# Performance work log

Hardware: AMD Instinct MI355X
Metric: run time of the kernel (lower is better)

Reference implementation:

```python
import jax, jax.numpy as jnp
import numpy as np

B = 64            # number of graphs
NODES_PER_G = 64  # real nodes per graph
N_MAX = 128       # max_num_nodes (dense padding)
NT = B * NODES_PER_G   # 4096 total nodes
E = 65536         # edges (and pairs)
H = 64            # hidden_dim
D_NODE = 32
POLY = 16


def setup_inputs() -> dict:
    key = jax.random.key(0)
    ks = jax.random.split(key, 12)
    node_x = jax.random.normal(ks[0], (NT, D_NODE), dtype=jnp.float32)
    loop_x = jax.random.normal(ks[1], (NT, POLY), dtype=jnp.float32)
    edge_attr = jax.random.normal(ks[2], (E, D_NODE), dtype=jnp.float32)
    pair_x = jax.random.normal(ks[3], (E, POLY), dtype=jnp.float32)
    W_node = jax.random.normal(ks[4], (D_NODE, H), dtype=jnp.float32) / np.sqrt(D_NODE)
    W_loop = jax.random.normal(ks[5], (POLY, H), dtype=jnp.float32) / np.sqrt(POLY)
    W_edge = jax.random.normal(ks[6], (D_NODE, H), dtype=jnp.float32) / np.sqrt(D_NODE)
    W_pair = jax.random.normal(ks[7], (POLY, H), dtype=jnp.float32) / np.sqrt(POLY)
    # sorted graph assignment: 64 nodes per graph
    batch = (jnp.arange(NT, dtype=jnp.int32) // NODES_PER_G).astype(jnp.int32)
    # intra-graph edges: global index = graph*NODES_PER_G + local
    epg = E // B  # edges per graph
    eg = (jnp.arange(E, dtype=jnp.int32) // epg)
    e_loc = jax.random.randint(ks[8], (2, E), 0, NODES_PER_G, dtype=jnp.int32)
    edge_index = eg[None, :] * NODES_PER_G + e_loc
    p_loc = jax.random.randint(ks[9], (2, E), 0, NODES_PER_G, dtype=jnp.int32)
    pair_index = eg[None, :] * NODES_PER_G + p_loc
    return {
        "node_x": node_x, "loop_x": loop_x, "edge_attr": edge_attr, "pair_x": pair_x,
        "W_node": W_node, "W_loop": W_loop, "W_edge": W_edge, "W_pair": W_pair,
        "batch": batch, "edge_index": edge_index, "pair_index": pair_index,
    }


def _positions(batch):
    # position of each node within its graph (to_dense_batch semantics)
    counts = jax.ops.segment_sum(jnp.ones_like(batch), batch, num_segments=B)
    starts = jnp.concatenate([jnp.zeros((1,), counts.dtype), jnp.cumsum(counts)[:-1]])
    return jnp.arange(batch.shape[0], dtype=batch.dtype) - starts[batch].astype(batch.dtype)


def _to_dense_adj(index, batch, pos, h):
    b = batch[index[0]]
    r = pos[index[0]]
    c = pos[index[1]]
    dense = jnp.zeros((B, N_MAX, N_MAX, H), dtype=h.dtype)
    return dense.at[b, r, c].add(h)  # duplicates are summed, as in to_dense_adj


def reference(node_x, loop_x, edge_attr, pair_x, W_node, W_loop, W_edge, W_pair,
              batch, edge_index, pair_index):
    pos = _positions(batch)
    # node + loop encoders (linear), then scatter to dense batch [B, N, H]
    node_h = node_x @ W_node + loop_x @ W_loop
    dense_node_h = jnp.zeros((B, N_MAX, H), dtype=node_h.dtype).at[batch, pos].set(node_h)
    dense_node_mask = jnp.zeros((B, N_MAX), dtype=bool).at[batch, pos].set(True)
    # permute (0,2,1) -> [B, H, N], then diag_embed -> [B, H, N, N]
    dnh = jnp.transpose(dense_node_h, (0, 2, 1))
    ar = jnp.arange(N_MAX)
    dense_diag_h = jnp.zeros((B, H, N_MAX, N_MAX), dtype=dnh.dtype).at[:, :, ar, ar].set(dnh)
    # edge + pair encoders, scatter to dense adjacency [B, N, N, H]
    edge_h = edge_attr @ W_edge
    pair_h = pair_x @ W_pair
    dense_pair = _to_dense_adj(edge_index, batch, pos, edge_h) \
               + _to_dense_adj(pair_index, batch, pos, pair_h)
    # permute (0,3,1,2) -> [B, H, N, N], add diagonal node features
    dense_pair_h = jnp.transpose(dense_pair, (0, 3, 1, 2)) + dense_diag_h
    return dense_pair_h, dense_node_mask
```

## Files before the change

kernel.cpp:

```cpp
#include <hip/hip_runtime.h>

#define NTOT  4096
#define NG    64
#define NMAXD 128
#define HD    64
#define NEDGE 65536
#define EPG   (NEDGE / NG)
#define NPG   (NTOT / NG)

typedef float f4 __attribute__((ext_vector_type(4)));

__device__ __forceinline__ int lowb(const int* __restrict__ batch, int key) {
  int lo = 0, hi = NTOT;
  while (lo < hi) { const int mid = (lo + hi) >> 1;
    if (batch[mid] < key) lo = mid + 1; else hi = mid; }
  return lo;
}

__global__ __launch_bounds__(256) void prep_all_kernel(
    const int* __restrict__ eI, const int* __restrict__ pI,
    const int* __restrict__ batch,
    int* __restrict__ rcE, int* __restrict__ rcP, int* __restrict__ rcN,
    int* __restrict__ counts) {
  const int i = blockIdx.x * 256 + threadIdx.x;
  if (i < NEDGE) {
    const int n0 = eI[i], n1 = eI[NEDGE + i];
    const int b0 = batch[n0], b1 = batch[n1];
    rcE[i] = (b0 << 16) | ((n0 - lowb(batch, b0)) << 8) | (n1 - lowb(batch, b1));
  } else if (i < 2 * NEDGE) {
    const int j = i - NEDGE;
    const int n0 = pI[j], n1 = pI[NEDGE + j];
    const int b0 = batch[n0], b1 = batch[n1];
    rcP[j] = (b0 << 16) | ((n0 - lowb(batch, b0)) << 8) | (n1 - lowb(batch, b1));
  } else if (i < 2 * NEDGE + NTOT) {
    const int j = i - 2 * NEDGE;
    const int b = batch[j];
    const int p = j - lowb(batch, b);
    rcN[j] = (b << 16) | (p << 8) | p;
  } else if (i < 2 * NEDGE + NTOT + NG) {
    const int g = i - 2 * NEDGE - NTOT;
    counts[g] = lowb(batch, g + 1) - lowb(batch, g);
  }
}

#define HQ 4
#define SCT 512
__global__ __launch_bounds__(SCT) void fused_scatter_kernel(
    const float* __restrict__ node_x, const float* __restrict__ loop_x,
    const float* __restrict__ edge_attr, const float* __restrict__ pair_x,
    const float* __restrict__ Wn, const float* __restrict__ Wl,
    const float* __restrict__ We, const float* __restrict__ Wp,
    const int* __restrict__ rcE, const int* __restrict__ rcP,
    const int* __restrict__ rcN, const int* __restrict__ counts,
    float* __restrict__ out, float* __restrict__ mask) {
  __shared__ float acc[HQ * 4096];
  __shared__ f4 WcE[32];
  __shared__ f4 WcP[16];
  __shared__ f4 WcN[48];

  const int tid = threadIdx.x;
  const int d  = (int)blockIdx.x;
  const int g  = ((d & 7) << 3) | ((d >> 3) & 7);
  const int h0 = (d >> 6) * HQ;

  if (tid < 32)       WcE[tid]            = *(const f4*)&We[tid * HD + h0];
  else if (tid < 48)  WcP[tid - 32]       = *(const f4*)&Wp[(tid - 32) * HD + h0];
  else if (tid < 80)  WcN[tid - 48]       = *(const f4*)&Wn[(tid - 48) * HD + h0];
  else if (tid < 96)  WcN[32 + tid - 80]  = *(const f4*)&Wl[(tid - 80) * HD + h0];
  for (int i = tid; i < HQ * 1024; i += SCT) ((f4*)acc)[i] = (f4)(0.f);
  __syncthreads();

  const int wid = tid >> 6;
  if (wid >= 4) {
    const int tz = tid - 256;
#pragma unroll
    for (int t = 0; t < HQ; ++t) {
      f4* plane = (f4*)(out + ((size_t)g * HD + h0 + t) * NMAXD * NMAXD);
#pragma unroll
      for (int k = 0; k < 4; ++k) {
        const int idx = tz + k * 256;
        plane[(idx >> 4) * 32 + 16 + (idx & 15)] = (f4)(0.f);
      }
#pragma unroll
      for (int k = 0; k < 8; ++k)
        plane[2048 + tz + k * 256] = (f4)(0.f);
    }
    if (h0 == 0) {
      const int cg = counts[g];
      for (int i = tz; i < NMAXD; i += 256)
        mask[(size_t)g * NMAXD + i] = (i < cg) ? 1.0f : 0.0f;
    }
  } else {
#pragma unroll
    for (int k = 0; k < 4; ++k) {
      const int j = g * EPG + tid + k * 256;
      const f4* xr = (const f4*)(edge_attr + (size_t)j * 32);
      f4 d4 = (f4)(0.f);
#pragma unroll
      for (int k4 = 0; k4 < 8; ++k4) {
        const f4 x = xr[k4];
#pragma unroll
        for (int u = 0; u < 4; ++u) d4 += x[u] * WcE[k4 * 4 + u];
      }
      const int code = rcE[j];
      const int b = code >> 16, r = (code >> 8) & 255, c = code & 255;
      if (b == g && r < 64 && c < 64) {
        const int a = r * 64 + c;
        unsafeAtomicAdd(&acc[a], d4.x);          unsafeAtomicAdd(&acc[4096 + a], d4.y);
        unsafeAtomicAdd(&acc[8192 + a], d4.z);   unsafeAtomicAdd(&acc[12288 + a], d4.w);
      } else {
        unsafeAtomicAdd(&out[(((size_t)b * HD + h0 + 0) * NMAXD + r) * NMAXD + c], d4.x);
        unsafeAtomicAdd(&out[(((size_t)b * HD + h0 + 1) * NMAXD + r) * NMAXD + c], d4.y);
        unsafeAtomicAdd(&out[(((size_t)b * HD + h0 + 2) * NMAXD + r) * NMAXD + c], d4.z);
        unsafeAtomicAdd(&out[(((size_t)b * HD + h0 + 3) * NMAXD + r) * NMAXD + c], d4.w);
      }
    }

#pragma unroll
    for (int k = 0; k < 4; ++k) {
      const int j = g * EPG + tid + k * 256;
      const f4* xr = (const f4*)(pair_x + (size_t)j * 16);
      f4 d4 = (f4)(0.f);
#pragma unroll
      for (int k4 = 0; k4 < 4; ++k4) {
        const f4 x = xr[k4];
#pragma unroll
        for (int u = 0; u < 4; ++u) d4 += x[u] * WcP[k4 * 4 + u];
      }
      const int code = rcP[j];
      const int b = code >> 16, r = (code >> 8) & 255, c = code & 255;
      if (b == g && r < 64 && c < 64) {
        const int a = r * 64 + c;
        unsafeAtomicAdd(&acc[a], d4.x);          unsafeAtomicAdd(&acc[4096 + a], d4.y);
        unsafeAtomicAdd(&acc[8192 + a], d4.z);   unsafeAtomicAdd(&acc[12288 + a], d4.w);
      } else {
        unsafeAtomicAdd(&out[(((size_t)b * HD + h0 + 0) * NMAXD + r) * NMAXD + c], d4.x);
        unsafeAtomicAdd(&out[(((size_t)b * HD + h0 + 1) * NMAXD + r) * NMAXD + c], d4.y);
        unsafeAtomicAdd(&out[(((size_t)b * HD + h0 + 2) * NMAXD + r) * NMAXD + c], d4.z);
        unsafeAtomicAdd(&out[(((size_t)b * HD + h0 + 3) * NMAXD + r) * NMAXD + c], d4.w);
      }
    }

    if (tid < NPG) {
      const int j = g * NPG + tid;
      const f4* xr = (const f4*)(node_x + (size_t)j * 32);
      const f4* lr = (const f4*)(loop_x + (size_t)j * 16);
      f4 d4 = (f4)(0.f);
#pragma unroll
      for (int k4 = 0; k4 < 8; ++k4) {
        const f4 x = xr[k4];
#pragma unroll
        for (int u = 0; u < 4; ++u) d4 += x[u] * WcN[k4 * 4 + u];
      }
#pragma unroll
      for (int k4 = 0; k4 < 4; ++k4) {
        const f4 x = lr[k4];
#pragma unroll
        for (int u = 0; u < 4; ++u) d4 += x[u] * WcN[32 + k4 * 4 + u];
      }
      const int code = rcN[j];
      const int b = code >> 16, r = (code >> 8) & 255, c = code & 255;
      if (b == g && r < 64 && c < 64) {
        const int a = r * 64 + c;
        unsafeAtomicAdd(&acc[a], d4.x);          unsafeAtomicAdd(&acc[4096 + a], d4.y);
        unsafeAtomicAdd(&acc[8192 + a], d4.z);   unsafeAtomicAdd(&acc[12288 + a], d4.w);
      } else {
        unsafeAtomicAdd(&out[(((size_t)b * HD + h0 + 0) * NMAXD + r) * NMAXD + c], d4.x);
        unsafeAtomicAdd(&out[(((size_t)b * HD + h0 + 1) * NMAXD + r) * NMAXD + c], d4.y);
        unsafeAtomicAdd(&out[(((size_t)b * HD + h0 + 2) * NMAXD + r) * NMAXD + c], d4.z);
        unsafeAtomicAdd(&out[(((size_t)b * HD + h0 + 3) * NMAXD + r) * NMAXD + c], d4.w);
      }
    }
  }
  __syncthreads();

#pragma unroll
  for (int t = 0; t < HQ; ++t) {
    f4* plane = (f4*)(out + ((size_t)g * HD + h0 + t) * NMAXD * NMAXD);
#pragma unroll
    for (int k = 0; k < 2; ++k) {
      const int idx = tid + k * SCT;
      const int r = idx >> 4, c4 = idx & 15;
      plane[r * 32 + c4] = *(const f4*)&acc[t * 4096 + r * 64 + c4 * 4];
    }
  }
}

extern "C" void kernel_launch(void* const* d_in, const int* in_sizes, int n_in,
                              void* d_out, int out_size, void* d_ws, size_t ws_size,
                              hipStream_t stream) {
  const float* node_x    = (const float*)d_in[0];
  const float* loop_x    = (const float*)d_in[1];
  const float* edge_attr = (const float*)d_in[2];
  const float* pair_x    = (const float*)d_in[3];
  const float* W_node    = (const float*)d_in[4];
  const float* W_loop    = (const float*)d_in[5];
  const float* W_edge    = (const float*)d_in[6];
  const float* W_pair    = (const float*)d_in[7];
  const int*   batch     = (const int*)d_in[8];
  const int*   edge_index = (const int*)d_in[9];
  const int*   pair_index = (const int*)d_in[10];

  float* out  = (float*)d_out;
  float* mask = out + (size_t)NG * HD * NMAXD * NMAXD;

  int* rcE    = (int*)d_ws;
  int* rcP    = rcE + NEDGE;
  int* rcN    = rcP + NEDGE;
  int* counts = rcN + NTOT;

  const int prep_items = 2 * NEDGE + NTOT + NG;
  prep_all_kernel<<<(prep_items + 255) / 256, 256, 0, stream>>>(
      edge_index, pair_index, batch, rcE, rcP, rcN, counts);
  fused_scatter_kernel<<<NG * 16, SCT, 0, stream>>>(node_x, loop_x, edge_attr,
      pair_x, W_node, W_loop, W_edge, W_pair, rcE, rcP, rcN, counts, out, mask);
}
```

Measured before the change: 73.39 us.

## Move output zero-fill into prep kernel and use all threads for scatter

```diff
diff --git a/kernel.cpp b/kernel.cpp
--- a/kernel.cpp
+++ b/kernel.cpp
@@ -10,6 +10,10 @@
 
 typedef float f4 __attribute__((ext_vector_type(4)));
 
+#define NZBLK 2048
+#define PREP_ITEMS (2 * NEDGE + NTOT + NG)
+#define NPBLK ((PREP_ITEMS + 255) / 256)
+
 __device__ __forceinline__ int lowb(const int* __restrict__ batch, int key) {
   int lo = 0, hi = NTOT;
   while (lo < hi) { const int mid = (lo + hi) >> 1;
@@ -17,12 +21,30 @@
   return lo;
 }
 
-__global__ __launch_bounds__(256) void prep_all_kernel(
+__global__ __launch_bounds__(256) void zero_prep_kernel(
     const int* __restrict__ eI, const int* __restrict__ pI,
     const int* __restrict__ batch,
     int* __restrict__ rcE, int* __restrict__ rcP, int* __restrict__ rcN,
-    int* __restrict__ counts) {
-  const int i = blockIdx.x * 256 + threadIdx.x;
+    int* __restrict__ counts, float* __restrict__ out) {
+  const int blk = (int)blockIdx.x;
+  const int tid = threadIdx.x;
+
+  if (blk < NZBLK) {
+#pragma unroll
+    for (int t = 0; t < 2; ++t) {
+      f4* plane = (f4*)(out + (size_t)(blk * 2 + t) * (NMAXD * NMAXD));
+#pragma unroll
+      for (int k = 0; k < 8; ++k) plane[2048 + tid + k * 256] = (f4)(0.f);
+#pragma unroll
+      for (int k = 0; k < 4; ++k) {
+        const int i = tid + k * 256;
+        plane[(i >> 4) * 32 + 16 + (i & 15)] = (f4)(0.f);
+      }
+    }
+    return;
+  }
+
+  const int i = (blk - NZBLK) * 256 + tid;
   if (i < NEDGE) {
     const int n0 = eI[i], n1 = eI[NEDGE + i];
     const int b0 = batch[n0], b1 = batch[n1];
@@ -37,15 +59,15 @@
     const int b = batch[j];
     const int p = j - lowb(batch, b);
     rcN[j] = (b << 16) | (p << 8) | p;
-  } else if (i < 2 * NEDGE + NTOT + NG) {
+  } else if (i < PREP_ITEMS) {
     const int g = i - 2 * NEDGE - NTOT;
     counts[g] = lowb(batch, g + 1) - lowb(batch, g);
   }
 }
 
 #define HQ 4
-#define SCT 512
-__global__ __launch_bounds__(SCT) void fused_scatter_kernel(
+#define BT 512
+__global__ __launch_bounds__(BT) void acc_kernel(
     const float* __restrict__ node_x, const float* __restrict__ loop_x,
     const float* __restrict__ edge_attr, const float* __restrict__ pair_x,
     const float* __restrict__ Wn, const float* __restrict__ Wl,
@@ -67,109 +89,87 @@
   else if (tid < 48)  WcP[tid - 32]       = *(const f4*)&Wp[(tid - 32) * HD + h0];
   else if (tid < 80)  WcN[tid - 48]       = *(const f4*)&Wn[(tid - 48) * HD + h0];
   else if (tid < 96)  WcN[32 + tid - 80]  = *(const f4*)&Wl[(tid - 80) * HD + h0];
-  for (int i = tid; i < HQ * 1024; i += SCT) ((f4*)acc)[i] = (f4)(0.f);
+  for (int i = tid; i < HQ * 1024; i += BT) ((f4*)acc)[i] = (f4)(0.f);
   __syncthreads();
 
-  const int wid = tid >> 6;
-  if (wid >= 4) {
-    const int tz = tid - 256;
-#pragma unroll
-    for (int t = 0; t < HQ; ++t) {
-      f4* plane = (f4*)(out + ((size_t)g * HD + h0 + t) * NMAXD * NMAXD);
-#pragma unroll
-      for (int k = 0; k < 4; ++k) {
-        const int idx = tz + k * 256;
-        plane[(idx >> 4) * 32 + 16 + (idx & 15)] = (f4)(0.f);
-      }
-#pragma unroll
-      for (int k = 0; k < 8; ++k)
-        plane[2048 + tz + k * 256] = (f4)(0.f);
-    }
-    if (h0 == 0) {
-      const int cg = counts[g];
-      for (int i = tz; i < NMAXD; i += 256)
-        mask[(size_t)g * NMAXD + i] = (i < cg) ? 1.0f : 0.0f;
-    }
-  } else {
-#pragma unroll
-    for (int k = 0; k < 4; ++k) {
-      const int j = g * EPG + tid + k * 256;
-      const f4* xr = (const f4*)(edge_attr + (size_t)j * 32);
-      f4 d4 = (f4)(0.f);
-#pragma unroll
-      for (int k4 = 0; k4 < 8; ++k4) {
-        const f4 x = xr[k4];
-#pragma unroll
-        for (int u = 0; u < 4; ++u) d4 += x[u] * WcE[k4 * 4 + u];
-      }
-      const int code = rcE[j];
-      const int b = code >> 16, r = (code >> 8) & 255, c = code & 255;
-      if (b == g && r < 64 && c < 64) {
-        const int a = r * 64 + c;
-        unsafeAtomicAdd(&acc[a], d4.x);          unsafeAtomicAdd(&acc[4096 + a], d4.y);
-        unsafeAtomicAdd(&acc[8192 + a], d4.z);   unsafeAtomicAdd(&acc[12288 + a], d4.w);
-      } else {
-        unsafeAtomicAdd(&out[(((size_t)b * HD + h0 + 0) * NMAXD + r) * NMAXD + c], d4.x);
-        unsafeAtomicAdd(&out[(((size_t)b * HD + h0 + 1) * NMAXD + r) * NMAXD + c], d4.y);
-        unsafeAtomicAdd(&out[(((size_t)b * HD + h0 + 2) * NMAXD + r) * NMAXD + c], d4.z);
-        unsafeAtomicAdd(&out[(((size_t)b * HD + h0 + 3) * NMAXD + r) * NMAXD + c], d4.w);
-      }
-    }
-
-#pragma unroll
-    for (int k = 0; k < 4; ++k) {
-      const int j = g * EPG + tid + k * 256;
-      const f4* xr = (const f4*)(pair_x + (size_t)j * 16);
-      f4 d4 = (f4)(0.f);
-#pragma unroll
-      for (int k4 = 0; k4 < 4; ++k4) {
-        const f4 x = xr[k4];
-#pragma unroll
-        for (int u = 0; u < 4; ++u) d4 += x[u] * WcP[k4 * 4 + u];
-      }
-      const int code = rcP[j];
-      const int b = code >> 16, r = (code >> 8) & 255, c = code & 255;
-      if (b == g && r < 64 && c < 64) {
-        const int a = r * 64 + c;
-        unsafeAtomicAdd(&acc[a], d4.x);          unsafeAtomicAdd(&acc[4096 + a], d4.y);
-        unsafeAtomicAdd(&acc[8192 + a], d4.z);   unsafeAtomicAdd(&acc[12288 + a], d4.w);
-      } else {
-        unsafeAtomicAdd(&out[(((size_t)b * HD + h0 + 0) * NMAXD + r) * NMAXD + c], d4.x);
-        unsafeAtomicAdd(&out[(((size_t)b * HD + h0 + 1) * NMAXD + r) * NMAXD + c], d4.y);
-        unsafeAtomicAdd(&out[(((size_t)b * HD + h0 + 2) * NMAXD + r) * NMAXD + c], d4.z);
-        unsafeAtomicAdd(&out[(((size_t)b * HD + h0 + 3) * NMAXD + r) * NMAXD + c], d4.w);
-      }
-    }
-
-    if (tid < NPG) {
-      const int j = g * NPG + tid;
-      const f4* xr = (const f4*)(node_x + (size_t)j * 32);
-      const f4* lr = (const f4*)(loop_x + (size_t)j * 16);
-      f4 d4 = (f4)(0.f);
-#pragma unroll
-      for (int k4 = 0; k4 < 8; ++k4) {
-        const f4 x = xr[k4];
-#pragma unroll
-        for (int u = 0; u < 4; ++u) d4 += x[u] * WcN[k4 * 4 + u];
-      }
-#pragma unroll
-      for (int k4 = 0; k4 < 4; ++k4) {
-        const f4 x = lr[k4];
-#pragma unroll
-        for (int u = 0; u < 4; ++u) d4 += x[u] * WcN[32 + k4 * 4 + u];
-      }
-      const int code = rcN[j];
-      const int b = code >> 16, r = (code >> 8) & 255, c = code & 255;
-      if (b == g && r < 64 && c < 64) {
-        const int a = r * 64 + c;
-        unsafeAtomicAdd(&acc[a], d4.x);          unsafeAtomicAdd(&acc[4096 + a], d4.y);
-        unsafeAtomicAdd(&acc[8192 + a], d4.z);   unsafeAtomicAdd(&acc[12288 + a], d4.w);
-      } else {
-        unsafeAtomicAdd(&out[(((size_t)b * HD + h0 + 0) * NMAXD + r) * NMAXD + c], d4.x);
-        unsafeAtomicAdd(&out[(((size_t)b * HD + h0 + 1) * NMAXD + r) * NMAXD + c], d4.y);
-        unsafeAtomicAdd(&out[(((size_t)b * HD + h0 + 2) * NMAXD + r) * NMAXD + c], d4.z);
-        unsafeAtomicAdd(&out[(((size_t)b * HD + h0 + 3) * NMAXD + r) * NMAXD + c], d4.w);
-      }
+#pragma unroll
+  for (int k = 0; k < 2; ++k) {
+    const int j = g * EPG + tid + k * BT;
+    const f4* xr = (const f4*)(edge_attr + (size_t)j * 32);
+    f4 d4 = (f4)(0.f);
+#pragma unroll
+    for (int k4 = 0; k4 < 8; ++k4) {
+      const f4 x = xr[k4];
+#pragma unroll
+      for (int u = 0; u < 4; ++u) d4 += x[u] * WcE[k4 * 4 + u];
+    }
+    const int code = rcE[j];
+    const int b = code >> 16, r = (code >> 8) & 255, c = code & 255;
+    if (b == g && r < 64 && c < 64) {
+      const int a = r * 64 + c;
+      unsafeAtomicAdd(&acc[a], d4.x);          unsafeAtomicAdd(&acc[4096 + a], d4.y);
+      unsafeAtomicAdd(&acc[8192 + a], d4.z);   unsafeAtomicAdd(&acc[12288 + a], d4.w);
+    } else {
+      unsafeAtomicAdd(&out[(((size_t)b * HD + h0 + 0) * NMAXD + r) * NMAXD + c], d4.x);
+      unsafeAtomicAdd(&out[(((size_t)b * HD + h0 + 1) * NMAXD + r) * NMAXD + c], d4.y);
+      unsafeAtomicAdd(&out[(((size_t)b * HD + h0 + 2) * NMAXD + r) * NMAXD + c], d4.z);
+      unsafeAtomicAdd(&out[(((size_t)b * HD + h0 + 3) * NMAXD + r) * NMAXD + c], d4.w);
+    }
+  }
+
+#pragma unroll
+  for (int k = 0; k < 2; ++k) {
+    const int j = g * EPG + tid + k * BT;
+    const f4* xr = (const f4*)(pair_x + (size_t)j * 16);
+    f4 d4 = (f4)(0.f);
+#pragma unroll
+    for (int k4 = 0; k4 < 4; ++k4) {
+      const f4 x = xr[k4];
+#pragma unroll
+      for (int u = 0; u < 4; ++u) d4 += x[u] * WcP[k4 * 4 + u];
+    }
+    const int code = rcP[j];
+    const int b = code >> 16, r = (code >> 8) & 255, c = code & 255;
+    if (b == g && r < 64 && c < 64) {
+      const int a = r * 64 + c;
+      unsafeAtomicAdd(&acc[a], d4.x);          unsafeAtomicAdd(&acc[4096 + a], d4.y);
+      unsafeAtomicAdd(&acc[8192 + a], d4.z);   unsafeAtomicAdd(&acc[12288 + a], d4.w);
+    } else {
+      unsafeAtomicAdd(&out[(((size_t)b * HD + h0 + 0) * NMAXD + r) * NMAXD + c], d4.x);
+      unsafeAtomicAdd(&out[(((size_t)b * HD + h0 + 1) * NMAXD + r) * NMAXD + c], d4.y);
+      unsafeAtomicAdd(&out[(((size_t)b * HD + h0 + 2) * NMAXD + r) * NMAXD + c], d4.z);
+      unsafeAtomicAdd(&out[(((size_t)b * HD + h0 + 3) * NMAXD + r) * NMAXD + c], d4.w);
+    }
+  }
+
+  if (tid < NPG) {
+    const int j = g * NPG + tid;
+    const f4* xr = (const f4*)(node_x + (size_t)j * 32);
+    const f4* lr = (const f4*)(loop_x + (size_t)j * 16);
+    f4 d4 = (f4)(0.f);
+#pragma unroll
+    for (int k4 = 0; k4 < 8; ++k4) {
+      const f4 x = xr[k4];
+#pragma unroll
+      for (int u = 0; u < 4; ++u) d4 += x[u] * WcN[k4 * 4 + u];
+    }
+#pragma unroll
+    for (int k4 = 0; k4 < 4; ++k4) {
+      const f4 x = lr[k4];
+#pragma unroll
+      for (int u = 0; u < 4; ++u) d4 += x[u] * WcN[32 + k4 * 4 + u];
+    }
+    const int code = rcN[j];
+    const int b = code >> 16, r = (code >> 8) & 255, c = code & 255;
+    if (b == g && r < 64 && c < 64) {
+      const int a = r * 64 + c;
+      unsafeAtomicAdd(&acc[a], d4.x);          unsafeAtomicAdd(&acc[4096 + a], d4.y);
+      unsafeAtomicAdd(&acc[8192 + a], d4.z);   unsafeAtomicAdd(&acc[12288 + a], d4.w);
+    } else {
+      unsafeAtomicAdd(&out[(((size_t)b * HD + h0 + 0) * NMAXD + r) * NMAXD + c], d4.x);
+      unsafeAtomicAdd(&out[(((size_t)b * HD + h0 + 1) * NMAXD + r) * NMAXD + c], d4.y);
+      unsafeAtomicAdd(&out[(((size_t)b * HD + h0 + 2) * NMAXD + r) * NMAXD + c], d4.z);
+      unsafeAtomicAdd(&out[(((size_t)b * HD + h0 + 3) * NMAXD + r) * NMAXD + c], d4.w);
     }
   }
   __syncthreads();
@@ -179,11 +179,14 @@
     f4* plane = (f4*)(out + ((size_t)g * HD + h0 + t) * NMAXD * NMAXD);
 #pragma unroll
     for (int k = 0; k < 2; ++k) {
-      const int idx = tid + k * SCT;
+      const int idx = tid + k * BT;
       const int r = idx >> 4, c4 = idx & 15;
       plane[r * 32 + c4] = *(const f4*)&acc[t * 4096 + r * 64 + c4 * 4];
     }
   }
+
+  if (h0 == 0 && tid < NMAXD)
+    mask[(size_t)g * NMAXD + tid] = (tid < counts[g]) ? 1.0f : 0.0f;
 }
 
 extern "C" void kernel_launch(void* const* d_in, const int* in_sizes, int n_in,
@@ -209,9 +212,8 @@
   int* rcN    = rcP + NEDGE;
   int* counts = rcN + NTOT;
 
-  const int prep_items = 2 * NEDGE + NTOT + NG;
-  prep_all_kernel<<<(prep_items + 255) / 256, 256, 0, stream>>>(
-      edge_index, pair_index, batch, rcE, rcP, rcN, counts);
-  fused_scatter_kernel<<<NG * 16, SCT, 0, stream>>>(node_x, loop_x, edge_attr,
+  zero_prep_kernel<<<NZBLK + NPBLK, 256, 0, stream>>>(
+      edge_index, pair_index, batch, rcE, rcP, rcN, counts, out);
+  acc_kernel<<<NG * 16, BT, 0, stream>>>(node_x, loop_x, edge_attr,
       pair_x, W_node, W_loop, W_edge, W_pair, rcE, rcP, rcN, counts, out, mask);
 }
```

Result: slower. 98.80 us (+34.6%).

## Split edge dot-products across 4 lanes with shuffle reduction and rotated LDS planes

Applied to the files above, without the earlier changes.

```diff
diff --git a/kernel.cpp b/kernel.cpp
--- a/kernel.cpp
+++ b/kernel.cpp
@@ -9,6 +9,15 @@
 #define NPG   (NTOT / NG)
 
 typedef float f4 __attribute__((ext_vector_type(4)));
+
+#define ROT(a, s) (((a) + (s) * 8) & 4095)
+
+__device__ __forceinline__ f4 shfl_xor_f4(f4 v, int m) {
+  f4 r;
+  r.x = __shfl_xor(v.x, m); r.y = __shfl_xor(v.y, m);
+  r.z = __shfl_xor(v.z, m); r.w = __shfl_xor(v.w, m);
+  return r;
+}
 
 __device__ __forceinline__ int lowb(const int* __restrict__ batch, int key) {
   int lo = 0, hi = NTOT;
@@ -91,84 +100,84 @@
         mask[(size_t)g * NMAXD + i] = (i < cg) ? 1.0f : 0.0f;
     }
   } else {
-#pragma unroll
-    for (int k = 0; k < 4; ++k) {
-      const int j = g * EPG + tid + k * 256;
-      const f4* xr = (const f4*)(edge_attr + (size_t)j * 32);
-      f4 d4 = (f4)(0.f);
-#pragma unroll
-      for (int k4 = 0; k4 < 8; ++k4) {
-        const f4 x = xr[k4];
-#pragma unroll
-        for (int u = 0; u < 4; ++u) d4 += x[u] * WcE[k4 * 4 + u];
-      }
-      const int code = rcE[j];
-      const int b = code >> 16, r = (code >> 8) & 255, c = code & 255;
-      if (b == g && r < 64 && c < 64) {
-        const int a = r * 64 + c;
-        unsafeAtomicAdd(&acc[a], d4.x);          unsafeAtomicAdd(&acc[4096 + a], d4.y);
-        unsafeAtomicAdd(&acc[8192 + a], d4.z);   unsafeAtomicAdd(&acc[12288 + a], d4.w);
-      } else {
-        unsafeAtomicAdd(&out[(((size_t)b * HD + h0 + 0) * NMAXD + r) * NMAXD + c], d4.x);
-        unsafeAtomicAdd(&out[(((size_t)b * HD + h0 + 1) * NMAXD + r) * NMAXD + c], d4.y);
-        unsafeAtomicAdd(&out[(((size_t)b * HD + h0 + 2) * NMAXD + r) * NMAXD + c], d4.z);
-        unsafeAtomicAdd(&out[(((size_t)b * HD + h0 + 3) * NMAXD + r) * NMAXD + c], d4.w);
-      }
-    }
-
-#pragma unroll
-    for (int k = 0; k < 4; ++k) {
-      const int j = g * EPG + tid + k * 256;
-      const f4* xr = (const f4*)(pair_x + (size_t)j * 16);
-      f4 d4 = (f4)(0.f);
-#pragma unroll
-      for (int k4 = 0; k4 < 4; ++k4) {
-        const f4 x = xr[k4];
-#pragma unroll
-        for (int u = 0; u < 4; ++u) d4 += x[u] * WcP[k4 * 4 + u];
-      }
-      const int code = rcP[j];
-      const int b = code >> 16, r = (code >> 8) & 255, c = code & 255;
-      if (b == g && r < 64 && c < 64) {
-        const int a = r * 64 + c;
-        unsafeAtomicAdd(&acc[a], d4.x);          unsafeAtomicAdd(&acc[4096 + a], d4.y);
-        unsafeAtomicAdd(&acc[8192 + a], d4.z);   unsafeAtomicAdd(&acc[12288 + a], d4.w);
-      } else {
-        unsafeAtomicAdd(&out[(((size_t)b * HD + h0 + 0) * NMAXD + r) * NMAXD + c], d4.x);
-        unsafeAtomicAdd(&out[(((size_t)b * HD + h0 + 1) * NMAXD + r) * NMAXD + c], d4.y);
-        unsafeAtomicAdd(&out[(((size_t)b * HD + h0 + 2) * NMAXD + r) * NMAXD + c], d4.z);
-        unsafeAtomicAdd(&out[(((size_t)b * HD + h0 + 3) * NMAXD + r) * NMAXD + c], d4.w);
-      }
-    }
-
-    if (tid < NPG) {
-      const int j = g * NPG + tid;
+    const int la  = tid;
+    const int sub = la & 3;
+    const int grp = la >> 2;
+
+    {
+      f4 we[8];
+#pragma unroll
+      for (int kk = 0; kk < 8; ++kk) we[kk] = WcE[sub * 8 + kk];
+#pragma unroll 4
+      for (int p = 0; p < 16; ++p) {
+        const int j = g * EPG + p * 64 + grp;
+        const f4* xr = (const f4*)(edge_attr + (size_t)j * 32);
+        const f4 x0 = xr[sub * 2], x1 = xr[sub * 2 + 1];
+        f4 a4 = x0.x * we[0] + x0.y * we[1] + x0.z * we[2] + x0.w * we[3]
+              + x1.x * we[4] + x1.y * we[5] + x1.z * we[6] + x1.w * we[7];
+        a4 += shfl_xor_f4(a4, 1);
+        a4 += shfl_xor_f4(a4, 2);
+        const float val = (sub == 0) ? a4.x : (sub == 1) ? a4.y
+                        : (sub == 2) ? a4.z : a4.w;
+        const int code = rcE[j];
+        const int b = code >> 16, r = (code >> 8) & 255, c = code & 255;
+        if (b == g && r < 64 && c < 64) {
+          const int a = r * 64 + c;
+          unsafeAtomicAdd(&acc[sub * 4096 + ROT(a, sub)], val);
+        } else {
+          unsafeAtomicAdd(&out[(((size_t)b * HD + h0 + sub) * NMAXD + r) * NMAXD + c], val);
+        }
+      }
+    }
+
+    {
+      f4 wp[4];
+#pragma unroll
+      for (int kk = 0; kk < 4; ++kk) wp[kk] = WcP[sub * 4 + kk];
+#pragma unroll 4
+      for (int p = 0; p < 16; ++p) {
+        const int j = g * EPG + p * 64 + grp;
+        const f4 x = ((const f4*)(pair_x + (size_t)j * 16))[sub];
+        f4 a4 = x.x * wp[0] + x.y * wp[1] + x.z * wp[2] + x.w * wp[3];
+        a4 += shfl_xor_f4(a4, 1);
+        a4 += shfl_xor_f4(a4, 2);
+        const float val = (sub == 0) ? a4.x : (sub == 1) ? a4.y
+                        : (sub == 2) ? a4.z : a4.w;
+        const int code = rcP[j];
+        const int b = code >> 16, r = (code >> 8) & 255, c = code & 255;
+        if (b == g && r < 64 && c < 64) {
+          const int a = r * 64 + c;
+          unsafeAtomicAdd(&acc[sub * 4096 + ROT(a, sub)], val);
+        } else {
+          unsafeAtomicAdd(&out[(((size_t)b * HD + h0 + sub) * NMAXD + r) * NMAXD + c], val);
+        }
+      }
+    }
+
+    {
+      f4 wn[8], wl[4];
+#pragma unroll
+      for (int kk = 0; kk < 8; ++kk) wn[kk] = WcN[sub * 8 + kk];
+#pragma unroll
+      for (int kk = 0; kk < 4; ++kk) wl[kk] = WcN[32 + sub * 4 + kk];
+      const int j = g * NPG + grp;
       const f4* xr = (const f4*)(node_x + (size_t)j * 32);
-      const f4* lr = (const f4*)(loop_x + (size_t)j * 16);
-      f4 d4 = (f4)(0.f);
-#pragma unroll
-      for (int k4 = 0; k4 < 8; ++k4) {
-        const f4 x = xr[k4];
-#pragma unroll
-        for (int u = 0; u < 4; ++u) d4 += x[u] * WcN[k4 * 4 + u];
-      }
-#pragma unroll
-      for (int k4 = 0; k4 < 4; ++k4) {
-        const f4 x = lr[k4];
-#pragma unroll
-        for (int u = 0; u < 4; ++u) d4 += x[u] * WcN[32 + k4 * 4 + u];
-      }
+      const f4 x0 = xr[sub * 2], x1 = xr[sub * 2 + 1];
+      const f4 xl = ((const f4*)(loop_x + (size_t)j * 16))[sub];
+      f4 a4 = x0.x * wn[0] + x0.y * wn[1] + x0.z * wn[2] + x0.w * wn[3]
+            + x1.x * wn[4] + x1.y * wn[5] + x1.z * wn[6] + x1.w * wn[7]
+            + xl.x * wl[0] + xl.y * wl[1] + xl.z * wl[2] + xl.w * wl[3];
+      a4 += shfl_xor_f4(a4, 1);
+      a4 += shfl_xor_f4(a4, 2);
+      const float val = (sub == 0) ? a4.x : (sub == 1) ? a4.y
+                      : (sub == 2) ? a4.z : a4.w;
       const int code = rcN[j];
       const int b = code >> 16, r = (code >> 8) & 255, c = code & 255;
       if (b == g && r < 64 && c < 64) {
         const int a = r * 64 + c;
-        unsafeAtomicAdd(&acc[a], d4.x);          unsafeAtomicAdd(&acc[4096 + a], d4.y);
-        unsafeAtomicAdd(&acc[8192 + a], d4.z);   unsafeAtomicAdd(&acc[12288 + a], d4.w);
+        unsafeAtomicAdd(&acc[sub * 4096 + ROT(a, sub)], val);
       } else {
-        unsafeAtomicAdd(&out[(((size_t)b * HD + h0 + 0) * NMAXD + r) * NMAXD + c], d4.x);
-        unsafeAtomicAdd(&out[(((size_t)b * HD + h0 + 1) * NMAXD + r) * NMAXD + c], d4.y);
-        unsafeAtomicAdd(&out[(((size_t)b * HD + h0 + 2) * NMAXD + r) * NMAXD + c], d4.z);
-        unsafeAtomicAdd(&out[(((size_t)b * HD + h0 + 3) * NMAXD + r) * NMAXD + c], d4.w);
+        unsafeAtomicAdd(&out[(((size_t)b * HD + h0 + sub) * NMAXD + r) * NMAXD + c], val);
       }
     }
   }
@@ -181,7 +190,8 @@
     for (int k = 0; k < 2; ++k) {
       const int idx = tid + k * SCT;
       const int r = idx >> 4, c4 = idx & 15;
-      plane[r * 32 + c4] = *(const f4*)&acc[t * 4096 + r * 64 + c4 * 4];
+      const int o = (r * 64 + c4 * 4 + t * 8) & 4095;
+      plane[r * 32 + c4] = *(const f4*)&acc[t * 4096 + o];
     }
   }
 }
```

After: 100.6 us. +37.0%, slower.

## Fuse index preprocessing into scatter kernel using per-block graph start table

Applied to the files above, without the earlier changes.

```diff
diff --git a/kernel.cpp b/kernel.cpp
--- a/kernel.cpp
+++ b/kernel.cpp
@@ -17,46 +17,21 @@
   return lo;
 }
 
-__global__ __launch_bounds__(256) void prep_all_kernel(
-    const int* __restrict__ eI, const int* __restrict__ pI,
-    const int* __restrict__ batch,
-    int* __restrict__ rcE, int* __restrict__ rcP, int* __restrict__ rcN,
-    int* __restrict__ counts) {
-  const int i = blockIdx.x * 256 + threadIdx.x;
-  if (i < NEDGE) {
-    const int n0 = eI[i], n1 = eI[NEDGE + i];
-    const int b0 = batch[n0], b1 = batch[n1];
-    rcE[i] = (b0 << 16) | ((n0 - lowb(batch, b0)) << 8) | (n1 - lowb(batch, b1));
-  } else if (i < 2 * NEDGE) {
-    const int j = i - NEDGE;
-    const int n0 = pI[j], n1 = pI[NEDGE + j];
-    const int b0 = batch[n0], b1 = batch[n1];
-    rcP[j] = (b0 << 16) | ((n0 - lowb(batch, b0)) << 8) | (n1 - lowb(batch, b1));
-  } else if (i < 2 * NEDGE + NTOT) {
-    const int j = i - 2 * NEDGE;
-    const int b = batch[j];
-    const int p = j - lowb(batch, b);
-    rcN[j] = (b << 16) | (p << 8) | p;
-  } else if (i < 2 * NEDGE + NTOT + NG) {
-    const int g = i - 2 * NEDGE - NTOT;
-    counts[g] = lowb(batch, g + 1) - lowb(batch, g);
-  }
-}
-
 #define HQ 4
 #define SCT 512
-__global__ __launch_bounds__(SCT) void fused_scatter_kernel(
+__global__ __launch_bounds__(SCT) void fused_all_kernel(
     const float* __restrict__ node_x, const float* __restrict__ loop_x,
     const float* __restrict__ edge_attr, const float* __restrict__ pair_x,
     const float* __restrict__ Wn, const float* __restrict__ Wl,
     const float* __restrict__ We, const float* __restrict__ Wp,
-    const int* __restrict__ rcE, const int* __restrict__ rcP,
-    const int* __restrict__ rcN, const int* __restrict__ counts,
+    const int* __restrict__ eI, const int* __restrict__ pI,
+    const int* __restrict__ batch,
     float* __restrict__ out, float* __restrict__ mask) {
   __shared__ float acc[HQ * 4096];
   __shared__ f4 WcE[32];
   __shared__ f4 WcP[16];
   __shared__ f4 WcN[48];
+  __shared__ int starts_l[NG + 1];
 
   const int tid = threadIdx.x;
   const int d  = (int)blockIdx.x;
@@ -67,6 +42,8 @@
   else if (tid < 48)  WcP[tid - 32]       = *(const f4*)&Wp[(tid - 32) * HD + h0];
   else if (tid < 80)  WcN[tid - 48]       = *(const f4*)&Wn[(tid - 48) * HD + h0];
   else if (tid < 96)  WcN[32 + tid - 80]  = *(const f4*)&Wl[(tid - 80) * HD + h0];
+  else if (tid >= 128 && tid < 192) starts_l[tid - 128] = lowb(batch, tid - 128);
+  else if (tid == 192) starts_l[NG] = NTOT;
   for (int i = tid; i < HQ * 1024; i += SCT) ((f4*)acc)[i] = (f4)(0.f);
   __syncthreads();
 
@@ -86,24 +63,28 @@
         plane[2048 + tz + k * 256] = (f4)(0.f);
     }
     if (h0 == 0) {
-      const int cg = counts[g];
+      const int cg = starts_l[g + 1] - starts_l[g];
       for (int i = tz; i < NMAXD; i += 256)
         mask[(size_t)g * NMAXD + i] = (i < cg) ? 1.0f : 0.0f;
     }
   } else {
+    const int la = tid;
+
 #pragma unroll
     for (int k = 0; k < 4; ++k) {
-      const int j = g * EPG + tid + k * 256;
+      const int j = g * EPG + la + k * 256;
+      const int n0 = eI[j], n1 = eI[NEDGE + j];
       const f4* xr = (const f4*)(edge_attr + (size_t)j * 32);
       f4 d4 = (f4)(0.f);
 #pragma unroll
       for (int k4 = 0; k4 < 8; ++k4) {
         const f4 x = xr[k4];
-#pragma unroll
-        for (int u = 0; u < 4; ++u) d4 += x[u] * WcE[k4 * 4 + u];
+        d4 += x.x * WcE[k4 * 4 + 0] + x.y * WcE[k4 * 4 + 1]
+            + x.z * WcE[k4 * 4 + 2] + x.w * WcE[k4 * 4 + 3];
       }
-      const int code = rcE[j];
-      const int b = code >> 16, r = (code >> 8) & 255, c = code & 255;
+      const int b = batch[n0];
+      const int r = n0 - starts_l[b];
+      const int c = n1 - starts_l[batch[n1]];
       if (b == g && r < 64 && c < 64) {
         const int a = r * 64 + c;
         unsafeAtomicAdd(&acc[a], d4.x);          unsafeAtomicAdd(&acc[4096 + a], d4.y);
@@ -118,17 +99,19 @@
 
 #pragma unroll
     for (int k = 0; k < 4; ++k) {
-      const int j = g * EPG + tid + k * 256;
+      const int j = g * EPG + la + k * 256;
+      const int n0 = pI[j], n1 = pI[NEDGE + j];
       const f4* xr = (const f4*)(pair_x + (size_t)j * 16);
       f4 d4 = (f4)(0.f);
 #pragma unroll
       for (int k4 = 0; k4 < 4; ++k4) {
         const f4 x = xr[k4];
-#pragma unroll
-        for (int u = 0; u < 4; ++u) d4 += x[u] * WcP[k4 * 4 + u];
+        d4 += x.x * WcP[k4 * 4 + 0] + x.y * WcP[k4 * 4 + 1]
+            + x.z * WcP[k4 * 4 + 2] + x.w * WcP[k4 * 4 + 3];
       }
-      const int code = rcP[j];
-      const int b = code >> 16, r = (code >> 8) & 255, c = code & 255;
+      const int b = batch[n0];
+      const int r = n0 - starts_l[b];
+      const int c = n1 - starts_l[batch[n1]];
       if (b == g && r < 64 && c < 64) {
         const int a = r * 64 + c;
         unsafeAtomicAdd(&acc[a], d4.x);          unsafeAtomicAdd(&acc[4096 + a], d4.y);
@@ -141,34 +124,34 @@
       }
     }
 
-    if (tid < NPG) {
-      const int j = g * NPG + tid;
+    if (la < NPG) {
+      const int j = g * NPG + la;
       const f4* xr = (const f4*)(node_x + (size_t)j * 32);
       const f4* lr = (const f4*)(loop_x + (size_t)j * 16);
       f4 d4 = (f4)(0.f);
 #pragma unroll
       for (int k4 = 0; k4 < 8; ++k4) {
         const f4 x = xr[k4];
-#pragma unroll
-        for (int u = 0; u < 4; ++u) d4 += x[u] * WcN[k4 * 4 + u];
+        d4 += x.x * WcN[k4 * 4 + 0] + x.y * WcN[k4 * 4 + 1]
+            + x.z * WcN[k4 * 4 + 2] + x.w * WcN[k4 * 4 + 3];
       }
 #pragma unroll
       for (int k4 = 0; k4 < 4; ++k4) {
         const f4 x = lr[k4];
-#pragma unroll
-        for (int u = 0; u < 4; ++u) d4 += x[u] * WcN[32 + k4 * 4 + u];
+        d4 += x.x * WcN[32 + k4 * 4 + 0] + x.y * WcN[32 + k4 * 4 + 1]
+            + x.z * WcN[32 + k4 * 4 + 2] + x.w * WcN[32 + k4 * 4 + 3];
       }
-      const int code = rcN[j];
-      const int b = code >> 16, r = (code >> 8) & 255, c = code & 255;
-      if (b == g && r < 64 && c < 64) {
-        const int a = r * 64 + c;
+      const int b = batch[j];
+      const int r = j - starts_l[b];
+      if (b == g && r < 64) {
+        const int a = r * 64 + r;
         unsafeAtomicAdd(&acc[a], d4.x);          unsafeAtomicAdd(&acc[4096 + a], d4.y);
         unsafeAtomicAdd(&acc[8192 + a], d4.z);   unsafeAtomicAdd(&acc[12288 + a], d4.w);
       } else {
-        unsafeAtomicAdd(&out[(((size_t)b * HD + h0 + 0) * NMAXD + r) * NMAXD + c], d4.x);
-        unsafeAtomicAdd(&out[(((size_t)b * HD + h0 + 1) * NMAXD + r) * NMAXD + c], d4.y);
-        unsafeAtomicAdd(&out[(((size_t)b * HD + h0 + 2) * NMAXD + r) * NMAXD + c], d4.z);
-        unsafeAtomicAdd(&out[(((size_t)b * HD + h0 + 3) * NMAXD + r) * NMAXD + c], d4.w);
+        unsafeAtomicAdd(&out[(((size_t)b * HD + h0 + 0) * NMAXD + r) * NMAXD + r], d4.x);
+        unsafeAtomicAdd(&out[(((size_t)b * HD + h0 + 1) * NMAXD + r) * NMAXD + r], d4.y);
+        unsafeAtomicAdd(&out[(((size_t)b * HD + h0 + 2) * NMAXD + r) * NMAXD + r], d4.z);
+        unsafeAtomicAdd(&out[(((size_t)b * HD + h0 + 3) * NMAXD + r) * NMAXD + r], d4.w);
       }
     }
   }
@@ -204,14 +187,7 @@
   float* out  = (float*)d_out;
   float* mask = out + (size_t)NG * HD * NMAXD * NMAXD;
 
-  int* rcE    = (int*)d_ws;
-  int* rcP    = rcE + NEDGE;
-  int* rcN    = rcP + NEDGE;
-  int* counts = rcN + NTOT;
-
-  const int prep_items = 2 * NEDGE + NTOT + NG;
-  prep_all_kernel<<<(prep_items + 255) / 256, 256, 0, stream>>>(
-      edge_index, pair_index, batch, rcE, rcP, rcN, counts);
-  fused_scatter_kernel<<<NG * 16, SCT, 0, stream>>>(node_x, loop_x, edge_attr,
-      pair_x, W_node, W_loop, W_edge, W_pair, rcE, rcP, rcN, counts, out, mask);
+  fused_all_kernel<<<NG * 16, SCT, 0, stream>>>(node_x, loop_x, edge_attr,
+      pair_x, W_node, W_loop, W_edge, W_pair, edge_index, pair_index,
+      batch, out, mask);
 }
```

Result: slower. 87.33 us (+19.0%).
